# Performance work log

Measured on AMD Instinct MI355X. Metric: run time of the kernel, lower is better.

The kernel has to match this reference:

```python
import jax, jax.numpy as jnp
import numpy as np

D_MODEL = 1024
NUM_HEADS = 16
GROUP_SIZE = 4
NUM_GROUPS = NUM_HEADS // GROUP_SIZE  # 4
D_K = D_MODEL // NUM_HEADS            # 64
THETA = 10000.0
WINDOW = 512


def _rope(x, positions):
    # x: (..., t, d) with d even; interleaved-pair rotation, freq_i = theta^{-i/(d/2)}
    d = x.shape[-1]
    half = d // 2
    inv_freq = THETA ** (-jnp.arange(half, dtype=x.dtype) / half)          # (half,)
    ang = positions.astype(x.dtype)[:, None] * inv_freq[None, :]           # (t, half)
    cos, sin = jnp.cos(ang), jnp.sin(ang)
    x1, x2 = x[..., 0::2], x[..., 1::2]
    r1 = x1 * cos - x2 * sin
    r2 = x1 * sin + x2 * cos
    return jnp.stack([r1, r2], axis=-1).reshape(x.shape)


def setup_inputs() -> dict:
    key = jax.random.key(0)
    k1, k2, k3, k4, k5 = jax.random.split(key, 5)
    b, t = 2, 2048
    scale = 1.0 / np.sqrt(D_MODEL)
    return {
        "x": jax.random.normal(k1, (b, t, D_MODEL), dtype=jnp.float32),
        "WQ": jax.random.normal(k2, (D_MODEL, D_MODEL), dtype=jnp.float32) * scale,
        "WK": jax.random.normal(k3, (NUM_GROUPS * D_K, D_MODEL), dtype=jnp.float32) * scale,
        "WV": jax.random.normal(k4, (NUM_GROUPS * D_K, D_MODEL), dtype=jnp.float32) * scale,
        "WO": jax.random.normal(k5, (D_MODEL, D_MODEL), dtype=jnp.float32) * scale,
        "token_positions": jnp.arange(t, dtype=jnp.int32),
    }


def reference(x, WQ, WK, WV, WO, token_positions):
    b, t, _ = x.shape
    g, s, d = NUM_GROUPS, GROUP_SIZE, D_K
    # projections (Linear: y = x @ W^T, no bias)
    q = (x @ WQ.T).reshape(b, t, g, s, d).transpose(0, 2, 3, 1, 4)  # b g s t d
    k = (x @ WK.T).reshape(b, t, g, d).transpose(0, 2, 1, 3)        # b g t d
    v = (x @ WV.T).reshape(b, t, g, d).transpose(0, 2, 1, 3)        # b g t d
    q = _rope(q, token_positions)
    k = _rope(k, token_positions)
    # scores: kv heads shared across the s query heads of each group
    scores = jnp.einsum('bgsqd,bgkd->bgsqk', q, k) / jnp.sqrt(jnp.asarray(d, x.dtype))
    i = jnp.arange(t)[:, None]
    j = jnp.arange(t)[None, :]
    allowed = (i >= j) & (i - j <= WINDOW)  # causal sliding window
    scores = jnp.where(allowed, scores, -jnp.inf)
    probs = jax.nn.softmax(scores, axis=-1)
    out = jnp.einsum('bgsqk,bgkd->bgsqd', probs, v)                 # b g s t d
    out = out.transpose(0, 3, 1, 2, 4).reshape(b, t, D_MODEL)       # b t (g s d)
    return out @ WO.T
```

## Files before the change

### kernel.cpp

```cpp
#include <hip/hip_runtime.h>
#include <hip/hip_bf16.h>

typedef __bf16 bf16;
typedef __bf16 bf16x4 __attribute__((ext_vector_type(4)));
typedef __bf16 bf16x8 __attribute__((ext_vector_type(8)));
typedef float  floatx4 __attribute__((ext_vector_type(4)));

#define D_MODEL   1024
#define NUM_HEADS 16
#define NUM_GROUPS 4
#define DK        64
#define SEQ_T     2048
#define BATCH     2
#define M_ROWS    (BATCH*SEQ_T)
#define WINDOW    512
#define KV_DIM    (NUM_GROUPS*DK)
#define N_QKV     (D_MODEL + 2*KV_DIM)
#define QSCALE    0.1803368801111204f
#define FREQ_C    0.4152410118609203f

#define GLDS16(g, l)                                                          \
    __builtin_amdgcn_global_load_lds(                                         \
        (const __attribute__((address_space(1))) void*)(g),                   \
        (__attribute__((address_space(3))) void*)(l), 16, 0, 0)

__global__ __launch_bounds__(256)
void convert_all(const float* s0, bf16* d0, int c0,
                 const float* s1, bf16* d1, int c1,
                 const float* s2, bf16* d2, int c2,
                 const float* s3, bf16* d3, int c3,
                 const float* s4, bf16* d4, int c4)
{
    int id = blockIdx.x * 256 + threadIdx.x;
    const float* src; bf16* dst;
    if      (id < c0)         { src = s0; dst = d0; }
    else if ((id -= c0) < c1) { src = s1; dst = d1; }
    else if ((id -= c1) < c2) { src = s2; dst = d2; }
    else if ((id -= c2) < c3) { src = s3; dst = d3; }
    else if ((id -= c3) < c4) { src = s4; dst = d4; }
    else return;
    int i = id * 8;
    const float* s = src + i;
    float4 a = *(const float4*)s;
    float4 b = *(const float4*)(s + 4);
    bf16x8 v;
    v[0] = (bf16)a.x; v[1] = (bf16)a.y; v[2] = (bf16)a.z; v[3] = (bf16)a.w;
    v[4] = (bf16)b.x; v[5] = (bf16)b.y; v[6] = (bf16)b.z; v[7] = (bf16)b.w;
    *(bf16x8*)&dst[i] = v;
}

__global__ __launch_bounds__(256, 3)
void gemm_t64(const bf16* __restrict__ A, const bf16* __restrict__ W, int K,
              bf16* __restrict__ Cq, bf16* __restrict__ Ck, bf16* __restrict__ Vt,
              float* __restrict__ Co, const int* __restrict__ pos, int mode)
{
    __shared__ bf16 As0[128 * 32], As1[128 * 32];
    __shared__ bf16 Bs0[64 * 32],  Bs1[64 * 32];

    const int tid  = threadIdx.x;
    const int wave = tid >> 6;
    const int lane = tid & 63;
    const int lr   = lane & 15;
    const int quad = lane >> 4;
    const int m0 = blockIdx.y * 128;
    const int n0 = blockIdx.x * 64;
    const int wm = (wave >> 1) * 64;
    const int wn = (wave & 1) * 32;

    const int srow = (lane >> 2);
    const int scol = (lane & 3) * 8;
    const bf16* Ap  = &A[(size_t)(m0 + wave * 16 + srow) * K + scol];
    const bf16* Ap2 = Ap + (size_t)64 * K;
    const bf16* Wp  = &W[(size_t)(n0 + wave * 16 + srow) * K + scol];
    bf16* As0a = &As0[wave * 512];
    bf16* As0b = &As0[2048 + wave * 512];
    bf16* As1a = &As1[wave * 512];
    bf16* As1b = &As1[2048 + wave * 512];
    bf16* Bs0d = &Bs0[wave * 512];
    bf16* Bs1d = &Bs1[wave * 512];

    floatx4 acc[4][2];
#pragma unroll
    for (int i = 0; i < 4; i++)
#pragma unroll
        for (int j = 0; j < 2; j++) acc[i][j] = (floatx4)(0.0f);

    for (int k0 = 0; k0 < K; k0 += 64) {
        __syncthreads();
        GLDS16(Ap  + k0,      As0a);
        GLDS16(Ap2 + k0,      As0b);
        GLDS16(Ap  + k0 + 32, As1a);
        GLDS16(Ap2 + k0 + 32, As1b);
        GLDS16(Wp  + k0,      Bs0d);
        GLDS16(Wp  + k0 + 32, Bs1d);
        __syncthreads();

        bf16x8 a0[4], a1[4], b0[2], b1[2];
#pragma unroll
        for (int mi = 0; mi < 4; mi++) {
            a0[mi] = *(const bf16x8*)&As0[(wm + mi * 16 + lr) * 32 + quad * 8];
            a1[mi] = *(const bf16x8*)&As1[(wm + mi * 16 + lr) * 32 + quad * 8];
        }
#pragma unroll
        for (int ni = 0; ni < 2; ni++) {
            b0[ni] = *(const bf16x8*)&Bs0[(wn + ni * 16 + lr) * 32 + quad * 8];
            b1[ni] = *(const bf16x8*)&Bs1[(wn + ni * 16 + lr) * 32 + quad * 8];
        }

#pragma unroll
        for (int mi = 0; mi < 4; mi++)
#pragma unroll
            for (int ni = 0; ni < 2; ni++) {
                acc[mi][ni] = __builtin_amdgcn_mfma_f32_16x16x32_bf16(
                    a0[mi], b0[ni], acc[mi][ni], 0, 0, 0);
                acc[mi][ni] = __builtin_amdgcn_mfma_f32_16x16x32_bf16(
                    a1[mi], b1[ni], acc[mi][ni], 0, 0, 0);
            }
    }

    if (mode == 0) {
        if (n0 >= D_MODEL + KV_DIM) {
            const int g  = (n0 - (D_MODEL + KV_DIM)) >> 6;
            const int b  = m0 >> 11;
            const int bg = b * 4 + g;
#pragma unroll
            for (int mi = 0; mi < 4; mi++) {
#pragma unroll
                for (int ni = 0; ni < 2; ni++) {
                    int d  = wn + ni * 16 + lr;
                    int t0 = (m0 & (SEQ_T - 1)) + wm + mi * 16 + quad * 4;
                    bf16x4 v;
#pragma unroll
                    for (int r = 0; r < 4; r++) v[r] = (bf16)acc[mi][ni][r];
                    *(bf16x4*)&Vt[((size_t)(bg * 64 + d)) * SEQ_T + t0] = v;
                }
            }
        } else {
            bf16* out; int ld, coff; float sc;
            if (n0 < D_MODEL) { out = Cq; ld = D_MODEL; coff = n0; sc = QSCALE; }
            else              { out = Ck; ld = KV_DIM;  coff = n0 - D_MODEL; sc = 1.0f; }
            float inv[2];
            float sgn = (lr & 1) ? 1.0f : -1.0f;
#pragma unroll
            for (int ni = 0; ni < 2; ni++) {
                int ip = (wn + ni * 16 + lr) >> 1;
                inv[ni] = exp2f(-(float)ip * FREQ_C);
            }
#pragma unroll
            for (int mi = 0; mi < 4; mi++) {
#pragma unroll
                for (int r = 0; r < 4; r++) {
                    int row = m0 + wm + mi * 16 + quad * 4 + r;
                    float p = (float)pos[row & (SEQ_T - 1)];
#pragma unroll
                    for (int ni = 0; ni < 2; ni++) {
                        float v  = acc[mi][ni][r];
                        float vp = __shfl_xor(v, 1);
                        float ang = p * inv[ni];
                        float ss, cc;
                        __sincosf(ang, &ss, &cc);
                        v = v * cc + vp * ss * sgn;
                        out[(size_t)row * ld + coff + wn + ni * 16 + lr] = (bf16)(v * sc);
                    }
                }
            }
        }
    } else {
#pragma unroll
        for (int mi = 0; mi < 4; mi++)
#pragma unroll
            for (int ni = 0; ni < 2; ni++)
#pragma unroll
                for (int r = 0; r < 4; r++) {
                    int row = m0 + wm + mi * 16 + quad * 4 + r;
                    int col = n0 + wn + ni * 16 + lr;
                    Co[(size_t)row * D_MODEL + col] = acc[mi][ni][r];
                }
    }
}

__global__ __launch_bounds__(256)
void attn_mfma(const bf16* __restrict__ Q, const bf16* __restrict__ K,
               const bf16* __restrict__ Vt_g, bf16* __restrict__ AO)
{
    const int ST = 72;
    __shared__ bf16 Ks[64 * ST];
    __shared__ bf16 Vt[80 * ST];
    __shared__ bf16 Ps[4 * 32 * ST];

    const int tid  = threadIdx.x;
    const int wave = tid >> 6;
    const int lane = tid & 63;
    const int lr   = lane & 15;
    const int quad = lane >> 4;
    const int bg = blockIdx.y;
    const int b = bg >> 2, g = bg & 3;
    const int h = g * 4 + wave;
    const int q0 = blockIdx.x * 32;

    bf16x8 qf[2][2];
#pragma unroll
    for (int mi = 0; mi < 2; mi++)
#pragma unroll
        for (int ks = 0; ks < 2; ks++)
            qf[mi][ks] = *(const bf16x8*)
                &Q[((size_t)(b * SEQ_T + q0 + mi * 16 + lr)) * D_MODEL
                   + h * 64 + ks * 32 + quad * 8];

    for (int i = tid; i < 15 * ST; i += 256) Vt[65 * ST + i] = (bf16)0.0f;
    if (tid < ST) Vt[64 * ST + tid] = (bf16)(tid < 64 ? 1.0f : 0.0f);

    bf16* Pw = &Ps[wave * 32 * ST];

    floatx4 o[2][5];
#pragma unroll
    for (int mi = 0; mi < 2; mi++)
#pragma unroll
        for (int nt = 0; nt < 5; nt++) o[mi][nt] = (floatx4)(0.0f);

    const int t0   = (q0 >= WINDOW) ? ((q0 - WINDOW) & ~63) : 0;
    const int last = q0 & ~63;

    for (int j0 = t0; j0 <= last; j0 += 64) {
        const bool mC = (j0 == last);
        const bool mW = (q0 >= WINDOW) && (j0 == t0);
        __syncthreads();
#pragma unroll
        for (int i = 0; i < 2; i++) {
            int c = tid + i * 256;
            int row = c >> 3, col8 = (c & 7) * 8;
            *(bf16x8*)&Ks[row * ST + col8] =
                *(const bf16x8*)&K[((size_t)(b * SEQ_T + j0 + row)) * KV_DIM + g * 64 + col8];
            *(bf16x8*)&Vt[row * ST + col8] =
                *(const bf16x8*)&Vt_g[((size_t)(bg * 64 + row)) * SEQ_T + j0 + col8];
        }
        __syncthreads();

        floatx4 s[2][4];
#pragma unroll
        for (int mi = 0; mi < 2; mi++)
#pragma unroll
            for (int nt = 0; nt < 4; nt++) s[mi][nt] = (floatx4)(0.0f);
#pragma unroll
        for (int ks = 0; ks < 2; ks++) {
#pragma unroll
            for (int nt = 0; nt < 4; nt++) {
                bf16x8 kf = *(const bf16x8*)&Ks[(nt * 16 + lr) * ST + ks * 32 + quad * 8];
                s[0][nt] = __builtin_amdgcn_mfma_f32_16x16x32_bf16(qf[0][ks], kf, s[0][nt], 0, 0, 0);
                s[1][nt] = __builtin_amdgcn_mfma_f32_16x16x32_bf16(qf[1][ks], kf, s[1][nt], 0, 0, 0);
            }
        }

        if (mC) {
#pragma unroll
            for (int mi = 0; mi < 2; mi++)
#pragma unroll
                for (int nt = 0; nt < 4; nt++) {
                    int key = j0 + nt * 16 + lr;
#pragma unroll
                    for (int r = 0; r < 4; r++) {
                        int qi_ = q0 + mi * 16 + quad * 4 + r;
                        s[mi][nt][r] = (key <= qi_) ? s[mi][nt][r] : -1e30f;
                    }
                }
        } else if (mW) {
#pragma unroll
            for (int mi = 0; mi < 2; mi++)
#pragma unroll
                for (int nt = 0; nt < 4; nt++) {
                    int key = j0 + nt * 16 + lr;
#pragma unroll
                    for (int r = 0; r < 4; r++) {
                        int qi_ = q0 + mi * 16 + quad * 4 + r;
                        s[mi][nt][r] = (qi_ - key <= WINDOW) ? s[mi][nt][r] : -1e30f;
                    }
                }
        }

#pragma unroll
        for (int mi = 0; mi < 2; mi++)
#pragma unroll
            for (int nt = 0; nt < 4; nt++)
#pragma unroll
                for (int r = 0; r < 4; r++)
                    Pw[(mi * 16 + quad * 4 + r) * ST + nt * 16 + lr] =
                        (bf16)exp2f(s[mi][nt][r]);

        __asm__ volatile("s_waitcnt lgkmcnt(0)" ::: "memory");

#pragma unroll
        for (int ks = 0; ks < 2; ks++) {
            bf16x8 pf0 = *(const bf16x8*)&Pw[(0 + lr) * ST + ks * 32 + quad * 8];
            bf16x8 pf1 = *(const bf16x8*)&Pw[(16 + lr) * ST + ks * 32 + quad * 8];
#pragma unroll
            for (int nt = 0; nt < 5; nt++) {
                bf16x8 vf = *(const bf16x8*)&Vt[(nt * 16 + lr) * ST + ks * 32 + quad * 8];
                o[0][nt] = __builtin_amdgcn_mfma_f32_16x16x32_bf16(pf0, vf, o[0][nt], 0, 0, 0);
                o[1][nt] = __builtin_amdgcn_mfma_f32_16x16x32_bf16(pf1, vf, o[1][nt], 0, 0, 0);
            }
        }
    }

#pragma unroll
    for (int mi = 0; mi < 2; mi++)
#pragma unroll
        for (int r = 0; r < 4; r++) {
            float l = __shfl(o[mi][4][r], lane & 48);
            float invl = 1.0f / l;
            int row = q0 + mi * 16 + quad * 4 + r;
#pragma unroll
            for (int nt = 0; nt < 4; nt++)
                AO[((size_t)(b * SEQ_T + row)) * D_MODEL + h * 64 + nt * 16 + lr] =
                    (bf16)(o[mi][nt][r] * invl);
        }
}

extern "C" void kernel_launch(void* const* d_in, const int* in_sizes, int n_in,
                              void* d_out, int out_size, void* d_ws, size_t ws_size,
                              hipStream_t stream)
{
    const float* x  = (const float*)d_in[0];
    const float* WQ = (const float*)d_in[1];
    const float* WK = (const float*)d_in[2];
    const float* WV = (const float*)d_in[3];
    const float* WO = (const float*)d_in[4];
    const int*  pos = (const int*)d_in[5];

    char* ws   = (char*)d_ws;
    bf16* Qw   = (bf16*)ws;
    bf16* Kw   = (bf16*)(ws + (size_t) 8 * 1024 * 1024);
    bf16* Vt_g = (bf16*)(ws + (size_t)10 * 1024 * 1024);
    bf16* xb   = (bf16*)(ws + (size_t)12 * 1024 * 1024);
    bf16* AO   = xb;
    bf16* Wqkv = (bf16*)(ws + (size_t)20 * 1024 * 1024);
    bf16* WOb  = (bf16*)(ws + (size_t)23 * 1024 * 1024);

    const int cx = (M_ROWS * D_MODEL) / 8;
    const int cq = (D_MODEL * D_MODEL) / 8;
    const int ck = (KV_DIM * D_MODEL) / 8;
    const int ctot = cx + cq + 2 * ck + cq;
    convert_all<<<ctot / 256, 256, 0, stream>>>(
        x, xb, cx,
        WQ, Wqkv, cq,
        WK, Wqkv + (size_t)D_MODEL * D_MODEL, ck,
        WV, Wqkv + (size_t)(D_MODEL + KV_DIM) * D_MODEL, ck,
        WO, WOb, cq);

    gemm_t64<<<dim3(N_QKV / 64, M_ROWS / 128), 256, 0, stream>>>(
        xb, Wqkv, D_MODEL, Qw, Kw, Vt_g, nullptr, pos, 0);

    attn_mfma<<<dim3(SEQ_T / 32, BATCH * NUM_GROUPS), 256, 0, stream>>>(
        Qw, Kw, Vt_g, AO);

    gemm_t64<<<dim3(D_MODEL / 64, M_ROWS / 128), 256, 0, stream>>>(
        AO, WOb, D_MODEL, nullptr, nullptr, nullptr, (float*)d_out, pos, 1);
}
```

Before: 149.5 us.

## Double-buffer LDS tiles in projection GEMM to overlap loads with MFMA

Turns the GEMM's shared-memory staging into a two-buffer ping-pong. The next K-tile is prefetched with global_load_lds while MFMAs run on the current tile, and there is one wait and barrier per iteration instead of two syncthreads. This is meant to hide global-load latency behind compute. LDS use doubles to about 48KB per block, which may limit the 3-blocks-per-CU occupancy target. Correctness relies on the end-of-iteration barrier stopping the next prefetch from overwriting a buffer that is still being read.

Measured after the change: 149.7 us. About the same (+0.1%).

```diff
diff --git a/kernel.cpp b/kernel.cpp
--- a/kernel.cpp
+++ b/kernel.cpp
@@ -54,8 +54,8 @@
               bf16* __restrict__ Cq, bf16* __restrict__ Ck, bf16* __restrict__ Vt,
               float* __restrict__ Co, const int* __restrict__ pos, int mode)
 {
-    __shared__ bf16 As0[128 * 32], As1[128 * 32];
-    __shared__ bf16 Bs0[64 * 32],  Bs1[64 * 32];
+    __shared__ bf16 As0[2][128 * 32], As1[2][128 * 32];
+    __shared__ bf16 Bs0[2][64 * 32],  Bs1[2][64 * 32];
 
     const int tid  = threadIdx.x;
     const int wave = tid >> 6;
@@ -72,12 +72,16 @@
     const bf16* Ap  = &A[(size_t)(m0 + wave * 16 + srow) * K + scol];
     const bf16* Ap2 = Ap + (size_t)64 * K;
     const bf16* Wp  = &W[(size_t)(n0 + wave * 16 + srow) * K + scol];
-    bf16* As0a = &As0[wave * 512];
-    bf16* As0b = &As0[2048 + wave * 512];
-    bf16* As1a = &As1[wave * 512];
-    bf16* As1b = &As1[2048 + wave * 512];
-    bf16* Bs0d = &Bs0[wave * 512];
-    bf16* Bs1d = &Bs1[wave * 512];
+
+#define STAGE(buf, kk)                                                        \
+    do {                                                                      \
+        GLDS16(Ap  + (kk),      &As0[buf][wave * 512]);                       \
+        GLDS16(Ap2 + (kk),      &As0[buf][2048 + wave * 512]);                \
+        GLDS16(Ap  + (kk) + 32, &As1[buf][wave * 512]);                       \
+        GLDS16(Ap2 + (kk) + 32, &As1[buf][2048 + wave * 512]);                \
+        GLDS16(Wp  + (kk),      &Bs0[buf][wave * 512]);                       \
+        GLDS16(Wp  + (kk) + 32, &Bs1[buf][wave * 512]);                      \
+    } while (0)
 
     floatx4 acc[4][2];
 #pragma unroll
@@ -85,26 +89,24 @@
 #pragma unroll
         for (int j = 0; j < 2; j++) acc[i][j] = (floatx4)(0.0f);
 
+    STAGE(0, 0);
+    __asm__ volatile("s_waitcnt vmcnt(0)" ::: "memory");
+    __builtin_amdgcn_s_barrier();
+
+    int cur = 0;
     for (int k0 = 0; k0 < K; k0 += 64) {
-        __syncthreads();
-        GLDS16(Ap  + k0,      As0a);
-        GLDS16(Ap2 + k0,      As0b);
-        GLDS16(Ap  + k0 + 32, As1a);
-        GLDS16(Ap2 + k0 + 32, As1b);
-        GLDS16(Wp  + k0,      Bs0d);
-        GLDS16(Wp  + k0 + 32, Bs1d);
-        __syncthreads();
+        if (k0 + 64 < K) STAGE(cur ^ 1, k0 + 64);
 
         bf16x8 a0[4], a1[4], b0[2], b1[2];
 #pragma unroll
         for (int mi = 0; mi < 4; mi++) {
-            a0[mi] = *(const bf16x8*)&As0[(wm + mi * 16 + lr) * 32 + quad * 8];
-            a1[mi] = *(const bf16x8*)&As1[(wm + mi * 16 + lr) * 32 + quad * 8];
+            a0[mi] = *(const bf16x8*)&As0[cur][(wm + mi * 16 + lr) * 32 + quad * 8];
+            a1[mi] = *(const bf16x8*)&As1[cur][(wm + mi * 16 + lr) * 32 + quad * 8];
         }
 #pragma unroll
         for (int ni = 0; ni < 2; ni++) {
-            b0[ni] = *(const bf16x8*)&Bs0[(wn + ni * 16 + lr) * 32 + quad * 8];
-            b1[ni] = *(const bf16x8*)&Bs1[(wn + ni * 16 + lr) * 32 + quad * 8];
+            b0[ni] = *(const bf16x8*)&Bs0[cur][(wn + ni * 16 + lr) * 32 + quad * 8];
+            b1[ni] = *(const bf16x8*)&Bs1[cur][(wn + ni * 16 + lr) * 32 + quad * 8];
         }
 
 #pragma unroll
@@ -116,7 +118,12 @@
                 acc[mi][ni] = __builtin_amdgcn_mfma_f32_16x16x32_bf16(
                     a1[mi], b1[ni], acc[mi][ni], 0, 0, 0);
             }
+
+        __asm__ volatile("s_waitcnt vmcnt(0)" ::: "memory");
+        __builtin_amdgcn_s_barrier();
+        cur ^= 1;
     }
+#undef STAGE
 
     if (mode == 0) {
         if (n0 >= D_MODEL + KV_DIM) {
```
